# Kernel optimization log

Hardware: AMD Instinct MI355X
Metric: run time of the kernel (lower is better)

Reference implementation:

```python
import jax, jax.numpy as jnp
import numpy as np

B, V, J = 65536, 4, 17  # frames, views, joints

def setup_inputs() -> dict:
    key = jax.random.key(0)
    k1, k2, k3 = jax.random.split(key, 3)
    points = jax.random.normal(k1, (B, V, J, 2), dtype=jnp.float32)
    confidences = jax.random.uniform(k2, (B, V, J), dtype=jnp.float32)
    proj_matricies = jax.random.normal(k3, (B, V, 3, 4), dtype=jnp.float32)
    return {"points": points, "confidences": confidences,
            "proj_matricies": proj_matricies, "batch": B}

def _triangulate(points, confidences, proj_matricies):
    # points: [B,V,J,2], confidences: [B,V,J], proj: [B,V,3,4]
    # DLT rows: conf * (x_i * P_row2 - P_row_i) for i in {0,1}
    P2 = proj_matricies[:, :, None, 2:3, :]          # [B,V,1,1,4]
    A = P2 * points[..., None]                        # [B,V,J,2,4]
    A = A - proj_matricies[:, :, None, 0:2, :]        # subtract rows 0,1
    A = A * confidences[..., None, None]              # [B,V,J,2,4]
    # gather per-joint matrices: [B,J,2V,4]
    A = jnp.transpose(A, (0, 2, 1, 3, 4)).reshape(A.shape[0], J, 2 * V, 4)
    _, _, vh = jnp.linalg.svd(A, full_matrices=False)  # vh: [B,J,4,4]
    homo = -vh[..., 3, :]                              # last right singular vector
    return homo[..., :3] / homo[..., 3:4]              # [B,J,3]

def reference(points, confidences, proj_matricies, batch):
    return _triangulate(points, confidences, proj_matricies)
```

## Files before the change

### kernel.cpp

```cpp
#include <hip/hip_runtime.h>
#include <cmath>

#pragma clang fp contract(off)


constexpr int BATCH  = 65536;
constexpr int VIEWS  = 4;
constexpr int JOINTS = 17;
constexpr int TOTAL  = BATCH * JOINTS;

#define EPS32  5.9604645e-08f
#define UNFL32 1.17549435e-38f

__device__ __forceinline__ float fsign(float a, float b) { return copysignf(a, b); }

__device__ __forceinline__ float frcp(float x)  { return __builtin_amdgcn_rcpf(x); }
__device__ __forceinline__ float frsq(float x)  { return __builtin_amdgcn_rsqf(x); }
__device__ __forceinline__ float fsqrtf(float x){ return __builtin_amdgcn_sqrtf(x); }


__device__ float snrm2_(const float* x, int n) {
    double s = 0.0;
    for (int i = 0; i < n; ++i) { double xi = (double)x[i]; s += xi * xi; }
    return (float)sqrt(s);
}

__device__ float slapy2_(float x, float y) {
    float xa = fabsf(x), ya = fabsf(y);
    float w = fmaxf(xa, ya), z = fminf(xa, ya);
    if (z == 0.0f) return w;
    float q = z / w;
    return w * __fsqrt_rn(1.0f + q * q);
}

__device__ float slarfg_(int n, float& alpha, float* x) {
    if (n <= 1) return 0.0f;
    float xnorm = snrm2_(x, n - 1);
    if (xnorm == 0.0f) return 0.0f;
    float beta = -fsign(slapy2_(alpha, xnorm), alpha);
    float tau  = (beta - alpha) / beta;
    float scal = 1.0f / (alpha - beta);
    for (int i = 0; i < n - 1; ++i) x[i] = scal * x[i];
    alpha = beta;
    return tau;
}

__device__ void slartg_(float f, float g, float& c, float& s, float& r) {
    if (g == 0.0f)      { c = 1.0f; s = 0.0f; r = f; }
    else if (f == 0.0f) { c = 0.0f; s = fsign(1.0f, g); r = fabsf(g); }
    else {
        float f1 = fabsf(f);
        float dd = __fsqrt_rn(f * f + g * g);
        c = f1 / dd;
        r = fsign(dd, f);
        s = g / r;
    }
}

__device__ void slas2_(float f, float g, float h, float& ssmin, float& ssmax) {
    float fa = fabsf(f), ga = fabsf(g), ha = fabsf(h);
    float fhmn = fminf(fa, ha), fhmx = fmaxf(fa, ha);
    if (fhmn == 0.0f) {
        ssmin = 0.0f;
        if (fhmx == 0.0f) ssmax = ga;
        else {
            float mn = fminf(fhmx, ga), mx = fmaxf(fhmx, ga);
            float q = mn / mx;
            ssmax = mx * __fsqrt_rn(1.0f + q * q);
        }
    } else {
        if (ga < fhmx) {
            float as_ = 1.0f + fhmn / fhmx;
            float at_ = (fhmx - fhmn) / fhmx;
            float q = ga / fhmx;
            float au = q * q;
            float cc = 2.0f / (__fsqrt_rn(as_ * as_ + au) + __fsqrt_rn(at_ * at_ + au));
            ssmin = fhmn * cc;
            ssmax = fhmx / cc;
        } else {
            float au = fhmx / ga;
            if (au == 0.0f) { ssmin = (fhmn * fhmx) / ga; ssmax = ga; }
            else {
                float as_ = 1.0f + fhmn / fhmx;
                float at_ = (fhmx - fhmn) / fhmx;
                float t1 = as_ * au, t2 = at_ * au;
                float cc = 1.0f / (__fsqrt_rn(1.0f + t1 * t1) + __fsqrt_rn(1.0f + t2 * t2));
                ssmin = (fhmn * cc) * au;
                ssmin = ssmin + ssmin;
                ssmax = ga / (cc + cc);
            }
        }
    }
}

__device__ void slasv2_(float f, float g, float h,
                        float& ssmin, float& ssmax,
                        float& snr, float& csr, float& snl, float& csl) {
    float ft = f, fa = fabsf(f), ht = h, ha = fabsf(h);
    int pmax = 1;
    bool swap = (ha > fa);
    if (swap) { pmax = 3; float t = ft; ft = ht; ht = t; t = fa; fa = ha; ha = t; }
    float gt = g, ga = fabsf(g);
    float clt = 0.0f, crt = 0.0f, slt = 0.0f, srt = 0.0f;
    if (ga == 0.0f) {
        ssmin = ha; ssmax = fa;
        clt = 1.0f; crt = 1.0f; slt = 0.0f; srt = 0.0f;
    } else {
        bool gasmal = true;
        if (ga > fa) {
            pmax = 2;
            if ((fa / ga) < EPS32) {
                gasmal = false;
                ssmax = ga;
                if (ha > 1.0f) ssmin = fa / (ga / ha);
                else           ssmin = (fa / ga) * ha;
                clt = 1.0f; slt = ht / gt;
                srt = 1.0f; crt = ft / gt;
            }
        }
        if (gasmal) {
            float dd = fa - ha;
            float l_ = (dd == fa) ? 1.0f : (dd / fa);
            float m_ = gt / ft;
            float t_ = 2.0f - l_;
            float mm = m_ * m_, tt = t_ * t_;
            float s_ = __fsqrt_rn(tt + mm);
            float r_ = (l_ == 0.0f) ? fabsf(m_) : __fsqrt_rn(l_ * l_ + mm);
            float a_ = 0.5f * (s_ + r_);
            ssmin = ha / a_;
            ssmax = fa * a_;
            if (mm == 0.0f) {
                if (l_ == 0.0f) t_ = fsign(2.0f, ft) * fsign(1.0f, gt);
                else            t_ = gt / fsign(dd, ft) + m_ / t_;
            } else {
                t_ = (m_ / (s_ + t_) + m_ / (r_ + l_)) * (1.0f + a_);
            }
            float ll = __fsqrt_rn(t_ * t_ + 4.0f);
            crt = 2.0f / ll;
            srt = t_ / ll;
            clt = (crt + srt * m_) / a_;
            slt = (ht / ft) * srt / a_;
        }
    }
    if (swap) { csl = srt; snl = crt; csr = slt; snr = clt; }
    else      { csl = clt; snl = slt; csr = crt; snr = srt; }
    float tsign = 0.0f;
    if (pmax == 1) tsign = fsign(1.0f, csr) * fsign(1.0f, csl) * fsign(1.0f, f);
    if (pmax == 2) tsign = fsign(1.0f, snr) * fsign(1.0f, csl) * fsign(1.0f, g);
    if (pmax == 3) tsign = fsign(1.0f, snr) * fsign(1.0f, snl) * fsign(1.0f, h);
    ssmax = fsign(ssmax, tsign);
    ssmin = fsign(ssmin, tsign * fsign(1.0f, f) * fsign(1.0f, h));
}

__device__ void sbdsqr4_(float* d, float* e, float VT[4][4]) {
    const float eps = EPS32, unfl = UNFL32;
    const float tol = 10.0f * eps;
    float thresh;
    {
        float sminoa = fabsf(d[0]);
        if (sminoa != 0.0f) {
            float mu = sminoa;
            for (int i = 1; i < 4; ++i) {
                mu = fabsf(d[i]) * (mu / (mu + fabsf(e[i - 1])));
                sminoa = fminf(sminoa, mu);
                if (sminoa == 0.0f) break;
            }
        }
        sminoa = sminoa / __fsqrt_rn(4.0f);
        thresh = fmaxf(tol * sminoa, 6.0f * (4.0f * (4.0f * unfl)));
    }
    int M = 4, oldll = -1000, oldm = -1000, idir = 0;
    float sminl = 0.0f;
    float rc[3], rs[3];
    for (int guard = 0; guard < 300 && M > 1; ++guard) {
        float smaxb = fabsf(d[M - 1]);
        int LLs = 0; bool defl = false, split = false;
        for (int lll = 1; lll <= M - 1; ++lll) {
            int ll = M - lll;
            float abse = fabsf(e[ll - 1]);
            float abss = fabsf(d[ll - 1]);
            if (abse <= thresh) {
                e[ll - 1] = 0.0f;
                if (ll == M - 1) { M = M - 1; defl = true; }
                else { LLs = ll; split = true; }
                break;
            }
            smaxb = fmaxf(fmaxf(smaxb, abss), abse);
        }
        if (defl) continue;
        int LL = (split ? LLs : 0) + 1;
        if (LL == M - 1) {
            float sigmn, sigmx, sinr, cosr, sinl, cosl;
            slasv2_(d[M - 2], e[M - 2], d[M - 1], sigmn, sigmx, sinr, cosr, sinl, cosl);
            d[M - 2] = sigmx; e[M - 2] = 0.0f; d[M - 1] = sigmn;
            for (int cc = 0; cc < 4; ++cc) {
                float st = cosr * VT[M - 2][cc] + sinr * VT[M - 1][cc];
                VT[M - 1][cc] = cosr * VT[M - 1][cc] - sinr * VT[M - 2][cc];
                VT[M - 2][cc] = st;
            }
            M -= 2;
            continue;
        }
        if (LL > oldm || M < oldll)
            idir = (fabsf(d[LL - 1]) >= fabsf(d[M - 1])) ? 1 : 2;
        bool cyc = false;
        if (idir == 1) {
            if (fabsf(e[M - 2]) <= tol * fabsf(d[M - 1])) { e[M - 2] = 0.0f; continue; }
            float mu = fabsf(d[LL - 1]); sminl = mu;
            for (int lll = LL; lll <= M - 1; ++lll) {
                if (fabsf(e[lll - 1]) <= tol * mu) { e[lll - 1] = 0.0f; cyc = true; break; }
                mu = fabsf(d[lll]) * (mu / (mu + fabsf(e[lll - 1])));
                sminl = fminf(sminl, mu);
            }
        } else {
            if (fabsf(e[LL - 1]) <= tol * fabsf(d[LL - 1])) { e[LL - 1] = 0.0f; continue; }
            float mu = fabsf(d[M - 1]); sminl = mu;
            for (int lll = M - 1; lll >= LL; --lll) {
                if (fabsf(e[lll - 1]) <= tol * mu) { e[lll - 1] = 0.0f; cyc = true; break; }
                mu = fabsf(d[lll - 1]) * (mu / (mu + fabsf(e[lll - 1])));
                sminl = fminf(sminl, mu);
            }
        }
        if (cyc) continue;
        oldll = LL; oldm = M;
        float shift = 0.0f;
        {
            float lhs = (4.0f * tol) * (sminl / smaxb);
            if (!(lhs <= fmaxf(eps, 0.01f * tol))) {
                float sll, rr2;
                if (idir == 1) { sll = fabsf(d[LL - 1]); slas2_(d[M - 2], e[M - 2], d[M - 1], shift, rr2); }
                else           { sll = fabsf(d[M - 1]); slas2_(d[LL - 1], e[LL - 1], d[LL], shift, rr2); }
                if (sll > 0.0f) {
                    float q = shift / sll;
                    if (q * q < eps) shift = 0.0f;
                }
            }
        }
        if (shift == 0.0f) {
            if (idir == 1) {
                float cs = 1.0f, oldcs = 1.0f, sn = 0.0f, oldsn = 0.0f, rr = 0.0f;
                for (int i = LL; i <= M - 1; ++i) {
                    float fv = d[i - 1] * cs;
                    slartg_(fv, e[i - 1], cs, sn, rr);
                    if (i > LL) e[i - 2] = oldsn * rr;
                    float fv2 = oldcs * rr;
                    float gv2 = d[i] * sn;
                    slartg_(fv2, gv2, oldcs, oldsn, d[i - 1]);
                    rc[i - LL] = cs; rs[i - LL] = sn;
                }
                float h = d[M - 1] * cs;
                d[M - 1] = h * oldcs;
                e[M - 2] = h * oldsn;
                for (int jj = 0; jj < M - LL; ++jj) {
                    float c = rc[jj], s = rs[jj];
                    if (c != 1.0f || s != 0.0f) {
                        int r0 = LL - 1 + jj;
                        for (int cc = 0; cc < 4; ++cc) {
                            float tmp = VT[r0 + 1][cc];
                            VT[r0 + 1][cc] = c * tmp - s * VT[r0][cc];
                            VT[r0][cc]     = s * tmp + c * VT[r0][cc];
                        }
                    }
                }
                if (fabsf(e[M - 2]) <= thresh) e[M - 2] = 0.0f;
            } else {
                float cs = 1.0f, oldcs = 1.0f, sn = 0.0f, oldsn = 0.0f, rr = 0.0f;
                for (int i = M; i >= LL + 1; --i) {
                    float fv = d[i - 1] * cs;
                    slartg_(fv, e[i - 2], cs, sn, rr);
                    if (i < M) e[i - 1] = oldsn * rr;
                    float fv2 = oldcs * rr;
                    float gv2 = d[i - 2] * sn;
                    slartg_(fv2, gv2, oldcs, oldsn, d[i - 1]);
                    rc[i - LL - 1] = oldcs; rs[i - LL - 1] = -oldsn;
                }
                float h = d[LL - 1] * cs;
                d[LL - 1] = h * oldcs;
                e[LL - 1] = h * oldsn;
                for (int jj = M - LL - 1; jj >= 0; --jj) {
                    float c = rc[jj], s = rs[jj];
                    if (c != 1.0f || s != 0.0f) {
                        int r0 = LL - 1 + jj;
                        for (int cc = 0; cc < 4; ++cc) {
                            float tmp = VT[r0 + 1][cc];
                            VT[r0 + 1][cc] = c * tmp - s * VT[r0][cc];
                            VT[r0][cc]     = s * tmp + c * VT[r0][cc];
                        }
                    }
                }
                if (fabsf(e[LL - 1]) <= thresh) e[LL - 1] = 0.0f;
            }
        } else {
            if (idir == 1) {
                float fv = (fabsf(d[LL - 1]) - shift) * (fsign(1.0f, d[LL - 1]) + shift / d[LL - 1]);
                float gv = e[LL - 1];
                float cosr, sinr, cosl, sinl, rr;
                for (int i = LL; i <= M - 1; ++i) {
                    slartg_(fv, gv, cosr, sinr, rr);
                    if (i > LL) e[i - 2] = rr;
                    fv = cosr * d[i - 1] + sinr * e[i - 1];
                    e[i - 1] = cosr * e[i - 1] - sinr * d[i - 1];
                    gv = sinr * d[i];
                    d[i] = cosr * d[i];
                    slartg_(fv, gv, cosl, sinl, rr);
                    d[i - 1] = rr;
                    fv = cosl * e[i - 1] + sinl * d[i];
                    d[i] = cosl * d[i] - sinl * e[i - 1];
                    if (i < M - 1) { gv = sinl * e[i]; e[i] = cosl * e[i]; }
                    rc[i - LL] = cosr; rs[i - LL] = sinr;
                }
                e[M - 2] = fv;
                for (int jj = 0; jj < M - LL; ++jj) {
                    float c = rc[jj], s = rs[jj];
                    if (c != 1.0f || s != 0.0f) {
                        int r0 = LL - 1 + jj;
                        for (int cc = 0; cc < 4; ++cc) {
                            float tmp = VT[r0 + 1][cc];
                            VT[r0 + 1][cc] = c * tmp - s * VT[r0][cc];
                            VT[r0][cc]     = s * tmp + c * VT[r0][cc];
                        }
                    }
                }
                if (fabsf(e[M - 2]) <= thresh) e[M - 2] = 0.0f;
            } else {
                float fv = (fabsf(d[M - 1]) - shift) * (fsign(1.0f, d[M - 1]) + shift / d[M - 1]);
                float gv = e[M - 2];
                float cosr, sinr, cosl, sinl, rr;
                for (int i = M; i >= LL + 1; --i) {
                    slartg_(fv, gv, cosr, sinr, rr);
                    if (i < M) e[i - 1] = rr;
                    fv = cosr * d[i - 1] + sinr * e[i - 2];
                    e[i - 2] = cosr * e[i - 2] - sinr * d[i - 1];
                    gv = sinr * d[i - 2];
                    d[i - 2] = cosr * d[i - 2];
                    slartg_(fv, gv, cosl, sinl, rr);
                    d[i - 1] = rr;
                    fv = cosl * e[i - 2] + sinl * d[i - 2];
                    d[i - 2] = cosl * d[i - 2] - sinl * e[i - 2];
                    if (i > LL + 1) { gv = sinl * e[i - 3]; e[i - 3] = cosl * e[i - 3]; }
                    rc[i - LL - 1] = cosl; rs[i - LL - 1] = -sinl;
                }
                e[LL - 1] = fv;
                if (fabsf(e[LL - 1]) <= thresh) e[LL - 1] = 0.0f;
                for (int jj = M - LL - 1; jj >= 0; --jj) {
                    float c = rc[jj], s = rs[jj];
                    if (c != 1.0f || s != 0.0f) {
                        int r0 = LL - 1 + jj;
                        for (int cc = 0; cc < 4; ++cc) {
                            float tmp = VT[r0 + 1][cc];
                            VT[r0 + 1][cc] = c * tmp - s * VT[r0][cc];
                            VT[r0][cc]     = s * tmp + c * VT[r0][cc];
                        }
                    }
                }
            }
        }
    }
    for (int i = 0; i < 4; ++i) {
        if (d[i] < 0.0f) {
            d[i] = -d[i];
            for (int cc = 0; cc < 4; ++cc) VT[i][cc] = -VT[i][cc];
        }
    }
    for (int i = 1; i <= 3; ++i) {
        int isub = 0; float smn = d[0];
        for (int jj = 1; jj <= 4 - i; ++jj)
            if (d[jj] <= smn) { isub = jj; smn = d[jj]; }
        int tgt = 4 - i;
        if (isub != tgt) {
            d[isub] = d[tgt]; d[tgt] = smn;
            for (int cc = 0; cc < 4; ++cc) {
                float t = VT[isub][cc]; VT[isub][cc] = VT[tgt][cc]; VT[tgt][cc] = t;
            }
        }
    }
}

__device__ __forceinline__ void build_A(const float* __restrict__ points,
                                        const float* __restrict__ confs,
                                        const float* __restrict__ proj,
                                        int b, int j, float Acm[4][8]) {
    #pragma unroll
    for (int v = 0; v < VIEWS; ++v) {
        int bv = b * VIEWS + v;
        const float4* Pq = (const float4*)(proj + (size_t)bv * 12);
        float4 P0 = Pq[0];
        float4 P1 = Pq[1];
        float4 P2 = Pq[2];
        float2 pt = *(const float2*)(points + ((size_t)bv * JOINTS + j) * 2);
        float  cf = confs[(size_t)bv * JOINTS + j];
        float p2[4] = {P2.x, P2.y, P2.z, P2.w};
        float p0[4] = {P0.x, P0.y, P0.z, P0.w};
        float p1[4] = {P1.x, P1.y, P1.z, P1.w};
        #pragma unroll
        for (int cc = 0; cc < 4; ++cc) {
            float r0 = (p2[cc] * pt.x) - p0[cc];
            float r1 = (p2[cc] * pt.y) - p1[cc];
            Acm[cc][2 * v + 0] = r0 * cf;
            Acm[cc][2 * v + 1] = r1 * cf;
        }
    }
}

__device__ void slow_solve(const float* __restrict__ points,
                           const float* __restrict__ confs,
                           const float* __restrict__ proj,
                           int b, int j, float& ox, float& oy, float& oz) {
    float Acm[4][8];
    build_A(points, confs, proj, b, j, Acm);

    for (int jc = 0; jc < 4; ++jc) {
        float alpha = Acm[jc][jc];
        float tau = slarfg_(8 - jc, alpha, &Acm[jc][jc + 1]);
        if (tau != 0.0f) {
            for (int c = jc + 1; c < 4; ++c) {
                float w = Acm[c][jc];
                for (int r = jc + 1; r < 8; ++r) w = w + Acm[jc][r] * Acm[c][r];
                float temp = -tau * w;
                Acm[c][jc] = Acm[c][jc] + temp;
                for (int r = jc + 1; r < 8; ++r) Acm[c][r] = Acm[c][r] + Acm[jc][r] * temp;
            }
        }
        Acm[jc][jc] = alpha;
    }

    float Rg[4][4];
    #pragma unroll
    for (int c = 0; c < 4; ++c)
        #pragma unroll
        for (int r = 0; r < 4; ++r)
            Rg[c][r] = (r <= c) ? Acm[c][r] : 0.0f;

    float d_[4], e_[4], taup[4];
    for (int i = 0; i < 4; ++i) {
        float alpha = Rg[i][i];
        float tau = slarfg_(4 - i, alpha, &Rg[i][i + 1]);
        d_[i] = alpha;
        if (tau != 0.0f) {
            for (int c = i + 1; c < 4; ++c) {
                float w = Rg[c][i];
                for (int r = i + 1; r < 4; ++r) w = w + Rg[i][r] * Rg[c][r];
                float temp = -tau * w;
                Rg[c][i] = Rg[c][i] + temp;
                for (int r = i + 1; r < 4; ++r) Rg[c][r] = Rg[c][r] + Rg[i][r] * temp;
            }
        }
        if (i < 3) {
            float alpha2 = Rg[i + 1][i];
            float xb[2]; int nt = 2 - i;
            for (int t = 0; t < nt && t < 2; ++t) xb[t] = Rg[i + 2 + t][i];
            float tau2 = slarfg_(3 - i, alpha2, xb);
            e_[i] = alpha2;
            for (int t = 0; t < nt && t < 2; ++t) Rg[i + 2 + t][i] = xb[t];
            taup[i] = tau2;
            if (tau2 != 0.0f) {
                for (int r = i + 1; r < 4; ++r) {
                    float w = Rg[i + 1][r];
                    for (int c = i + 2; c < 4; ++c) w = w + Rg[c][i] * Rg[c][r];
                    float ntau = -tau2;
                    Rg[i + 1][r] = Rg[i + 1][r] + w * ntau;
                    for (int c = i + 2; c < 4; ++c) {
                        float tc = ntau * Rg[c][i];
                        Rg[c][r] = Rg[c][r] + w * tc;
                    }
                }
            }
        } else taup[i] = 0.0f;
    }

    float VT[4][4] = {{1,0,0,0},{0,1,0,0},{0,0,1,0},{0,0,0,1}};
    sbdsqr4_(d_, e_, VT);

    for (int ii = 2; ii >= 0; --ii) {
        float tau = taup[ii];
        if (tau == 0.0f) continue;
        for (int r = 0; r < 4; ++r) {
            float w = VT[r][ii + 1];
            for (int c = ii + 2; c < 4; ++c) w = w + VT[r][c] * Rg[c][ii];
            float ntau = -tau;
            VT[r][ii + 1] = VT[r][ii + 1] + w * ntau;
            for (int c = ii + 2; c < 4; ++c) {
                float tc = ntau * Rg[c][ii];
                VT[r][c] = VT[r][c] + w * tc;
            }
        }
    }

    float w3 = VT[3][3];
    ox = VT[3][0] / w3;
    oy = VT[3][1] / w3;
    oz = VT[3][2] / w3;
}

__device__ __forceinline__ bool fast_solve(const float* __restrict__ points,
                                           const float* __restrict__ confs,
                                           const float* __restrict__ proj,
                                           int b, int j,
                                           float& ox, float& oy, float& oz) {
    float Acm[4][8];
    build_A(points, confs, proj, b, j, Acm);

    float M[4][4];
    #pragma unroll
    for (int c1 = 0; c1 < 4; ++c1) {
        #pragma unroll
        for (int c2 = c1; c2 < 4; ++c2) {
            float s = 0.0f;
            #pragma unroll
            for (int i = 0; i < 8; ++i)
                s = fmaf(Acm[c1][i], Acm[c2][i], s);
            M[c1][c2] = s;
        }
    }

    float V[4][4] = {{1,0,0,0},{0,1,0,0},{0,0,1,0},{0,0,0,1}};

    bool badconv = false;
    for (int sweep = 0; sweep < 6; ++sweep) {
        bool last = (sweep == 5);
        bool rot = false;
        #pragma unroll
        for (int p = 0; p < 3; ++p) {
            #pragma unroll
            for (int q = p + 1; q < 4; ++q) {
                float lp = M[p][p], lq = M[q][q], g = M[p][q];
                if (g * g > 1e-14f * (lp * lq)) {
                    rot = true;
                    float zeta = 0.5f * (lq - lp) * frcp(g);
                    float t  = fsign(frcp(fabsf(zeta) +
                                          fsqrtf(fmaf(zeta, zeta, 1.0f))), zeta);
                    if (last && fabsf(t) > 3e-4f) badconv = true;
                    float ci = frsq(fmaf(t, t, 1.0f));
                    float si = ci * t;
                    #pragma unroll
                    for (int k = 0; k < 4; ++k) {
                        if (k == p || k == q) continue;
                        float mpk = (k < p) ? M[k][p] : M[p][k];
                        float mqk = (k < q) ? M[k][q] : M[q][k];
                        float npk = fmaf(ci, mpk, -si * mqk);
                        float nqk = fmaf(si, mpk,  ci * mqk);
                        if (k < p) M[k][p] = npk; else M[p][k] = npk;
                        if (k < q) M[k][q] = nqk; else M[q][k] = nqk;
                    }
                    M[p][p] = fmaf(-t, g, lp);
                    M[q][q] = fmaf( t, g, lq);
                    M[p][q] = 0.0f;
                    #pragma unroll
                    for (int i = 0; i < 4; ++i) {
                        float vp = V[i][p], vq = V[i][q];
                        V[i][p] = fmaf(ci, vp, -si * vq);
                        V[i][q] = fmaf(si, vp,  ci * vq);
                    }
                }
            }
        }
        if (!__any((int)rot)) break;
    }

    float l0 = M[0][0], l1 = M[1][1], l2 = M[2][2], l3 = M[3][3];
    int idx = 0; float lm = l0;
    if (l1 < lm) { lm = l1; idx = 1; }
    if (l2 < lm) { lm = l2; idx = 2; }
    if (l3 < lm) { lm = l3; idx = 3; }

    float a0 = l0, a1 = l1, a2 = l2, a3 = l3;
    { float t;
      if (a0 > a1) { t = a0; a0 = a1; a1 = t; }
      if (a2 > a3) { t = a2; a2 = a3; a3 = t; }
      if (a0 > a2) { t = a0; a0 = a2; a2 = t; }
      if (a1 > a3) { t = a1; a1 = a3; a3 = t; }
      if (a1 > a2) { t = a1; a1 = a2; a2 = t; }
    }
    float lgap = fmaxf(a1 - a0, 0.0f);

    float hw  = V[3][idx];
    float inv = frcp(hw);
    ox = V[0][idx] * inv;
    oy = V[1][idx] * inv;
    oz = V[2][idx] * inv;

    float osq = fmaf(ox, ox, fmaf(oy, oy, oz * oz));
    float est = EPS32 * (a3 * frcp(lgap)) * (1.0f + osq);
    return !(est <= 1000.0f) || badconv;
}


__global__ __launch_bounds__(256) void triangulate_kernel(
    const float* __restrict__ points, const float* __restrict__ confs,
    const float* __restrict__ proj, float* __restrict__ out)
{
    int tid = blockIdx.x * blockDim.x + threadIdx.x;
    int b = tid / JOINTS;
    int j = tid - b * JOINTS;

    float ox, oy, oz;
    bool flag = fast_solve(points, confs, proj, b, j, ox, oy, oz);
    if (flag) slow_solve(points, confs, proj, b, j, ox, oy, oz);

    float* o = out + (size_t)tid * 3;
    o[0] = ox; o[1] = oy; o[2] = oz;
}

extern "C" void kernel_launch(void* const* d_in, const int* in_sizes, int n_in,
                              void* d_out, int out_size, void* d_ws, size_t ws_size,
                              hipStream_t stream) {
    const float* points = (const float*)d_in[0];
    const float* confs  = (const float*)d_in[1];
    const float* proj   = (const float*)d_in[2];
    float* out = (float*)d_out;

    dim3 block(256);
    dim3 grid((TOTAL + 255) / 256);
    triangulate_kernel<<<grid, block, 0, stream>>>(points, confs, proj, out);
}
```

Measured before the change: 176.3 us.

## Process two joint problems per thread with branchless interleaved Jacobi sweeps

Each thread now solves two independent 4x4 eigenproblems (indices tid and tid+HALF), interleaving their Jacobi rotations, and the grid is halved. Rotations are made branchless through selects, so both instances execute every rotation without divergent branches, which adds ILP and hides the latency of transcendental ops. The cost is higher register pressure, lower occupancy, extra work on skipped rotations, and both instances running until the slower one converges. The slow fallback path is still taken per instance.

```diff
diff --git a/kernel.cpp b/kernel.cpp
--- a/kernel.cpp
+++ b/kernel.cpp
@@ -8,6 +8,7 @@
 constexpr int VIEWS  = 4;
 constexpr int JOINTS = 17;
 constexpr int TOTAL  = BATCH * JOINTS;
+constexpr int HALF   = TOTAL / 2;
 
 #define EPS32  5.9604645e-08f
 #define UNFL32 1.17549435e-38f
@@ -492,30 +493,44 @@
     oz = VT[3][2] / w3;
 }
 
-__device__ __forceinline__ bool fast_solve(const float* __restrict__ points,
-                                           const float* __restrict__ confs,
-                                           const float* __restrict__ proj,
-                                           int b, int j,
-                                           float& ox, float& oy, float& oz) {
-    float Acm[4][8];
-    build_A(points, confs, proj, b, j, Acm);
-
-    float M[4][4];
-    #pragma unroll
-    for (int c1 = 0; c1 < 4; ++c1) {
+
+__global__ __launch_bounds__(256) void triangulate_kernel(
+    const float* __restrict__ points, const float* __restrict__ confs,
+    const float* __restrict__ proj, float* __restrict__ out)
+{
+    int tid = blockIdx.x * blockDim.x + threadIdx.x;
+    int t0 = tid;
+    int t1 = tid + HALF;
+
+    float M[2][4][4];
+    float V[2][4][4];
+    {
+        float Acm[4][8];
         #pragma unroll
-        for (int c2 = c1; c2 < 4; ++c2) {
-            float s = 0.0f;
+        for (int inst = 0; inst < 2; ++inst) {
+            int tt = inst ? t1 : t0;
+            int b = tt / JOINTS;
+            int j = tt - b * JOINTS;
+            build_A(points, confs, proj, b, j, Acm);
             #pragma unroll
-            for (int i = 0; i < 8; ++i)
-                s = fmaf(Acm[c1][i], Acm[c2][i], s);
-            M[c1][c2] = s;
-        }
-    }
-
-    float V[4][4] = {{1,0,0,0},{0,1,0,0},{0,0,1,0},{0,0,0,1}};
-
-    bool badconv = false;
+            for (int c1 = 0; c1 < 4; ++c1)
+                #pragma unroll
+                for (int c2 = c1; c2 < 4; ++c2) {
+                    float s = 0.0f;
+                    #pragma unroll
+                    for (int i = 0; i < 8; ++i)
+                        s = fmaf(Acm[c1][i], Acm[c2][i], s);
+                    M[inst][c1][c2] = s;
+                }
+            #pragma unroll
+            for (int r = 0; r < 4; ++r)
+                #pragma unroll
+                for (int c = 0; c < 4; ++c)
+                    V[inst][r][c] = (r == c) ? 1.0f : 0.0f;
+        }
+    }
+
+    bool badconv[2] = {false, false};
     for (int sweep = 0; sweep < 6; ++sweep) {
         bool last = (sweep == 5);
         bool rot = false;
@@ -523,33 +538,37 @@
         for (int p = 0; p < 3; ++p) {
             #pragma unroll
             for (int q = p + 1; q < 4; ++q) {
-                float lp = M[p][p], lq = M[q][q], g = M[p][q];
-                if (g * g > 1e-14f * (lp * lq)) {
-                    rot = true;
-                    float zeta = 0.5f * (lq - lp) * frcp(g);
-                    float t  = fsign(frcp(fabsf(zeta) +
-                                          fsqrtf(fmaf(zeta, zeta, 1.0f))), zeta);
-                    if (last && fabsf(t) > 3e-4f) badconv = true;
+                #pragma unroll
+                for (int inst = 0; inst < 2; ++inst) {
+                    float lp = M[inst][p][p], lq = M[inst][q][q], g = M[inst][p][q];
+                    bool cond = (g * g > 1e-14f * (lp * lq));
+                    rot |= cond;
+                    float gs = cond ? g : 1.0f;
+                    float zeta = 0.5f * (lq - lp) * frcp(gs);
+                    float t = fsign(frcp(fabsf(zeta) +
+                                         fsqrtf(fmaf(zeta, zeta, 1.0f))), zeta);
+                    t = cond ? t : 0.0f;
+                    badconv[inst] |= (last && fabsf(t) > 3e-4f);
                     float ci = frsq(fmaf(t, t, 1.0f));
                     float si = ci * t;
                     #pragma unroll
                     for (int k = 0; k < 4; ++k) {
                         if (k == p || k == q) continue;
-                        float mpk = (k < p) ? M[k][p] : M[p][k];
-                        float mqk = (k < q) ? M[k][q] : M[q][k];
+                        float mpk = (k < p) ? M[inst][k][p] : M[inst][p][k];
+                        float mqk = (k < q) ? M[inst][k][q] : M[inst][q][k];
                         float npk = fmaf(ci, mpk, -si * mqk);
                         float nqk = fmaf(si, mpk,  ci * mqk);
-                        if (k < p) M[k][p] = npk; else M[p][k] = npk;
-                        if (k < q) M[k][q] = nqk; else M[q][k] = nqk;
+                        if (k < p) M[inst][k][p] = npk; else M[inst][p][k] = npk;
+                        if (k < q) M[inst][k][q] = nqk; else M[inst][q][k] = nqk;
                     }
-                    M[p][p] = fmaf(-t, g, lp);
-                    M[q][q] = fmaf( t, g, lq);
-                    M[p][q] = 0.0f;
+                    M[inst][p][p] = fmaf(-t, g, lp);
+                    M[inst][q][q] = fmaf( t, g, lq);
+                    M[inst][p][q] = cond ? 0.0f : g;
                     #pragma unroll
                     for (int i = 0; i < 4; ++i) {
-                        float vp = V[i][p], vq = V[i][q];
-                        V[i][p] = fmaf(ci, vp, -si * vq);
-                        V[i][q] = fmaf(si, vp,  ci * vq);
+                        float vp = V[inst][i][p], vq = V[inst][i][q];
+                        V[inst][i][p] = fmaf(ci, vp, -si * vq);
+                        V[inst][i][q] = fmaf(si, vp,  ci * vq);
                     }
                 }
             }
@@ -557,48 +576,44 @@
         if (!__any((int)rot)) break;
     }
 
-    float l0 = M[0][0], l1 = M[1][1], l2 = M[2][2], l3 = M[3][3];
-    int idx = 0; float lm = l0;
-    if (l1 < lm) { lm = l1; idx = 1; }
-    if (l2 < lm) { lm = l2; idx = 2; }
-    if (l3 < lm) { lm = l3; idx = 3; }
-
-    float a0 = l0, a1 = l1, a2 = l2, a3 = l3;
-    { float t;
-      if (a0 > a1) { t = a0; a0 = a1; a1 = t; }
-      if (a2 > a3) { t = a2; a2 = a3; a3 = t; }
-      if (a0 > a2) { t = a0; a0 = a2; a2 = t; }
-      if (a1 > a3) { t = a1; a1 = a3; a3 = t; }
-      if (a1 > a2) { t = a1; a1 = a2; a2 = t; }
-    }
-    float lgap = fmaxf(a1 - a0, 0.0f);
-
-    float hw  = V[3][idx];
-    float inv = frcp(hw);
-    ox = V[0][idx] * inv;
-    oy = V[1][idx] * inv;
-    oz = V[2][idx] * inv;
-
-    float osq = fmaf(ox, ox, fmaf(oy, oy, oz * oz));
-    float est = EPS32 * (a3 * frcp(lgap)) * (1.0f + osq);
-    return !(est <= 1000.0f) || badconv;
-}
-
-
-__global__ __launch_bounds__(256) void triangulate_kernel(
-    const float* __restrict__ points, const float* __restrict__ confs,
-    const float* __restrict__ proj, float* __restrict__ out)
-{
-    int tid = blockIdx.x * blockDim.x + threadIdx.x;
-    int b = tid / JOINTS;
-    int j = tid - b * JOINTS;
-
-    float ox, oy, oz;
-    bool flag = fast_solve(points, confs, proj, b, j, ox, oy, oz);
-    if (flag) slow_solve(points, confs, proj, b, j, ox, oy, oz);
-
-    float* o = out + (size_t)tid * 3;
-    o[0] = ox; o[1] = oy; o[2] = oz;
+    #pragma unroll
+    for (int inst = 0; inst < 2; ++inst) {
+        float l0 = M[inst][0][0], l1 = M[inst][1][1];
+        float l2 = M[inst][2][2], l3 = M[inst][3][3];
+        int idx = 0; float lm = l0;
+        if (l1 < lm) { lm = l1; idx = 1; }
+        if (l2 < lm) { lm = l2; idx = 2; }
+        if (l3 < lm) { lm = l3; idx = 3; }
+
+        float a0 = l0, a1 = l1, a2 = l2, a3 = l3;
+        { float t;
+          if (a0 > a1) { t = a0; a0 = a1; a1 = t; }
+          if (a2 > a3) { t = a2; a2 = a3; a3 = t; }
+          if (a0 > a2) { t = a0; a0 = a2; a2 = t; }
+          if (a1 > a3) { t = a1; a1 = a3; a3 = t; }
+          if (a1 > a2) { t = a1; a1 = a2; a2 = t; }
+        }
+        float lgap = fmaxf(a1 - a0, 0.0f);
+
+        float hw  = V[inst][3][idx];
+        float inv = frcp(hw);
+        float ox = V[inst][0][idx] * inv;
+        float oy = V[inst][1][idx] * inv;
+        float oz = V[inst][2][idx] * inv;
+
+        float osq = fmaf(ox, ox, fmaf(oy, oy, oz * oz));
+        float est = EPS32 * (a3 * frcp(lgap)) * (1.0f + osq);
+        bool flag = !(est <= 1000.0f) || badconv[inst];
+
+        int tt = inst ? t1 : t0;
+        if (flag) {
+            int b = tt / JOINTS;
+            int j = tt - b * JOINTS;
+            slow_solve(points, confs, proj, b, j, ox, oy, oz);
+        }
+        float* o = out + (size_t)tt * 3;
+        o[0] = ox; o[1] = oy; o[2] = oz;
+    }
 }
 
 extern "C" void kernel_launch(void* const* d_in, const int* in_sizes, int n_in,
@@ -610,6 +625,6 @@
     float* out = (float*)d_out;
 
     dim3 block(256);
-    dim3 grid((TOTAL + 255) / 256);
+    dim3 grid(HALF / 256);
     triangulate_kernel<<<grid, block, 0, stream>>>(points, confs, proj, out);
 }
```

After: 184.1 us. 1.04x slower.
